# Kernel tuning notes

Hardware: AMD Instinct MI355X
Metric: run time of the kernel (lower is better)

The kernel has to match this reference:

```python
import jax, jax.numpy as jnp
import numpy as np
from jax import lax

KSIZE = 11
SIGMA = 1.5
C1 = (0.01 * 1.0) ** 2
C2 = (0.03 * 1.0) ** 2
PAD = (KSIZE - 1) // 2  # 5


def _gaussian_2d(ksize: int, sigma: float) -> np.ndarray:
    half = (ksize - 1) * 0.5
    g = np.exp(-0.5 * (np.linspace(-half, half, ksize) / sigma) ** 2)
    g = g / g.sum()
    return np.outer(g, g).astype(np.float32)  # [k, k]


def setup_inputs() -> dict:
    key = jax.random.key(0)
    kx, ky = jax.random.split(key)
    B, C, T, H, W = 2, 3, 8, 512, 512
    x = jax.random.uniform(kx, (B, C, T, H, W), dtype=jnp.float32)
    y = jax.random.uniform(ky, (B, C, T, H, W), dtype=jnp.float32)
    k2d = jnp.asarray(_gaussian_2d(KSIZE, SIGMA))
    # depthwise conv3d kernel: [C_out=C, C_in/groups=1, kD=1, kH, kW]
    kernel = jnp.broadcast_to(k2d[None, None, None], (C, 1, 1, KSIZE, KSIZE))
    return {"x": x, "y": y, "kernel": kernel}


def reference(x, y, kernel):
    C = x.shape[1]

    def conv(z):
        return lax.conv_general_dilated(
            z, kernel,
            window_strides=(1, 1, 1),
            padding=((0, 0), (PAD, PAD), (PAD, PAD)),
            dimension_numbers=("NCDHW", "OIDHW", "NCDHW"),
            feature_group_count=C,
        )

    # single grouped conv over the 5 stacked statistics, as in the original
    stacked = jnp.concatenate([x, y, x * x, y * y, x * y], axis=0)
    ux, uy, uxx, uyy, uxy = jnp.split(conv(stacked), 5, axis=0)

    vx = uxx - ux * ux
    vy = uyy - uy * uy
    vxy = uxy - ux * uy
    a1 = 2.0 * ux * uy + C1
    a2 = 2.0 * vxy + C2
    b1 = ux * ux + uy * uy + C1
    b2 = vx + vy + C2
    return a1 * a2 / (b1 * b2)
```

## Files before the change

kernel.cpp:

```cpp
#include <hip/hip_runtime.h>
#include <type_traits>

namespace {
constexpr int HH = 512;
constexpr int WW = 512;
constexpr int KS = 11;
constexpr int PADR = 5;
constexpr int TH = 32;
constexpr int TW = 64;
constexpr int SLAB = 16;
constexpr int HC = TW + 2 * PADR;
constexpr int LP = 77;
constexpr int NTHREADS = 256;
constexpr float SSIM_C1 = 1.0e-4f;
constexpr float SSIM_C2 = 9.0e-4f;
}

__global__ __launch_bounds__(NTHREADS, 4) void ssim_fused(
    const float* __restrict__ x, const float* __restrict__ y,
    const float* __restrict__ kern, float* __restrict__ out)
{
    __shared__ float vb[5][SLAB][LP];

    constexpr int tiles_w = WW / TW;
    constexpr int tiles_h = HH / TH;
    constexpr int tpp = tiles_w * tiles_h;

    const int bid = blockIdx.x;
    const int plane = bid / tpp;
    const int trem = bid - plane * tpp;
    const int tr_idx = trem / tiles_w;
    const int tile_r = tr_idx * TH;
    const int tile_c = (trem - tr_idx * tiles_w) * TW;

    const float* __restrict__ xp = x + (size_t)plane * (HH * WW);
    const float* __restrict__ yp = y + (size_t)plane * (HH * WW);
    float* __restrict__ op = out + (size_t)plane * (HH * WW);

    float wt[KS];
    {
        const float c = kern[5 * KS + 5];
        const float inv = rsqrtf(c);
#pragma unroll
        for (int i = 0; i < KS; ++i) wt[i] = kern[5 * KS + i] * inv;
    }

    const int t = threadIdx.x;
    const bool interior = (tile_r >= PADR) && (tile_r + TH + PADR <= HH) &&
                          (tile_c >= PADR) && (tile_c + TW + PADR <= WW);

    const int p2_r = t >> 4;
    const int p2_c0 = (t & 15) * 4;

    auto run_slab = [&](int s0, auto intr_tag) {
        constexpr bool INTR = decltype(intr_tag)::value;
        for (int i = t; i < SLAB * HC; i += NTHREADS) {
            const int r = i / HC;
            const int c = i - r * HC;
            const int gr = tile_r + s0 + r;
            const int gc = tile_c + c - PADR;
            float sx = 0.f, sy = 0.f, sxx = 0.f, syy = 0.f, sxy = 0.f;
            if (INTR) {
                const float* xq = xp + (gr - PADR) * WW + gc;
                const float* yq = yp + (gr - PADR) * WW + gc;
#pragma unroll
                for (int k = 0; k < KS; ++k) {
                    const float xv = xq[k * WW];
                    const float yv = yq[k * WW];
                    const float w = wt[k];
                    sx  += w * xv;
                    sy  += w * yv;
                    sxx += w * xv * xv;
                    syy += w * yv * yv;
                    sxy += w * xv * yv;
                }
            } else {
                const bool cok = (gc >= 0) & (gc < WW);
#pragma unroll
                for (int k = 0; k < KS; ++k) {
                    const int rr = gr - PADR + k;
                    const bool ok = cok & (rr >= 0) & (rr < HH);
                    float xv = 0.f, yv = 0.f;
                    if (ok) {
                        xv = xp[rr * WW + gc];
                        yv = yp[rr * WW + gc];
                    }
                    const float w = wt[k];
                    sx  += w * xv;
                    sy  += w * yv;
                    sxx += w * xv * xv;
                    syy += w * yv * yv;
                    sxy += w * xv * yv;
                }
            }
            vb[0][r][c] = sx;
            vb[1][r][c] = sy;
            vb[2][r][c] = sxx;
            vb[3][r][c] = syy;
            vb[4][r][c] = sxy;
        }
        __syncthreads();

        float res[5][4];
#pragma unroll
        for (int s = 0; s < 5; ++s) {
            float wnd[KS + 3];
#pragma unroll
            for (int i2 = 0; i2 < KS + 3; ++i2) wnd[i2] = vb[s][p2_r][p2_c0 + i2];
#pragma unroll
            for (int j = 0; j < 4; ++j) {
                float a = 0.f;
#pragma unroll
                for (int k = 0; k < KS; ++k) a += wt[k] * wnd[j + k];
                res[s][j] = a;
            }
        }
        float4 o;
#pragma unroll
        for (int j = 0; j < 4; ++j) {
            const float ux = res[0][j], uy = res[1][j];
            const float uxx = res[2][j], uyy = res[3][j], uxy = res[4][j];
            const float vx  = uxx - ux * ux;
            const float vy  = uyy - uy * uy;
            const float vxy = uxy - ux * uy;
            const float a1 = 2.f * ux * uy + SSIM_C1;
            const float a2 = 2.f * vxy + SSIM_C2;
            const float b1 = ux * ux + uy * uy + SSIM_C1;
            const float b2 = vx + vy + SSIM_C2;
            (&o.x)[j] = (a1 * a2) * __builtin_amdgcn_rcpf(b1 * b2);
        }
        *(float4*)(op + (size_t)(tile_r + s0 + p2_r) * WW + (tile_c + p2_c0)) = o;
        __syncthreads();
    };

    if (interior) {
        run_slab(0,    std::true_type{});
        run_slab(SLAB, std::true_type{});
    } else {
        run_slab(0,    std::false_type{});
        run_slab(SLAB, std::false_type{});
    }
}

extern "C" void kernel_launch(void* const* d_in, const int* in_sizes, int n_in,
                              void* d_out, int out_size, void* d_ws, size_t ws_size,
                              hipStream_t stream) {
    const float* x    = (const float*)d_in[0];
    const float* y    = (const float*)d_in[1];
    const float* kern = (const float*)d_in[2];
    float* out = (float*)d_out;

    const int nplanes = in_sizes[0] / (HH * WW);
    const int nblocks = nplanes * (HH / TH) * (WW / TW);

    ssim_fused<<<dim3(nblocks), dim3(NTHREADS), 0, stream>>>(x, y, kern, out);
}
```

Measured before the change: 227.3 us.

## Process full-width row bands with register sliding vertical blur

Blocks now each own a full-width band of 32 rows instead of a 32x64 tile. Each thread loads float2 columns and computes 8 output rows of the vertical pass from 18 input rows held in registers, so each input row is loaded once per round rather than 11 times per output. The horizontal halo is reduced to zero padding in shared memory. In exchange the grid shrinks to 768 blocks, register pressure rises (launch bounds drop to 3), and there are more barriers per block.

```diff
diff --git a/kernel.cpp b/kernel.cpp
--- a/kernel.cpp
+++ b/kernel.cpp
@@ -6,32 +6,25 @@
 constexpr int WW = 512;
 constexpr int KS = 11;
 constexpr int PADR = 5;
-constexpr int TH = 32;
-constexpr int TW = 64;
-constexpr int SLAB = 16;
-constexpr int HC = TW + 2 * PADR;
-constexpr int LP = 77;
+constexpr int BH = 32;
+constexpr int VR = 8;
+constexpr int SR = 4;
+constexpr int LP = 525;
 constexpr int NTHREADS = 256;
 constexpr float SSIM_C1 = 1.0e-4f;
 constexpr float SSIM_C2 = 9.0e-4f;
 }
 
-__global__ __launch_bounds__(NTHREADS, 4) void ssim_fused(
+__global__ __launch_bounds__(NTHREADS, 3) void ssim_fused(
     const float* __restrict__ x, const float* __restrict__ y,
     const float* __restrict__ kern, float* __restrict__ out)
 {
-    __shared__ float vb[5][SLAB][LP];
-
-    constexpr int tiles_w = WW / TW;
-    constexpr int tiles_h = HH / TH;
-    constexpr int tpp = tiles_w * tiles_h;
+    __shared__ float vb[5][SR][LP];
 
     const int bid = blockIdx.x;
-    const int plane = bid / tpp;
-    const int trem = bid - plane * tpp;
-    const int tr_idx = trem / tiles_w;
-    const int tile_r = tr_idx * TH;
-    const int tile_c = (trem - tr_idx * tiles_w) * TW;
+    const int plane = bid >> 4;
+    const int band  = bid & 15;
+    const int tile_r = band * BH;
 
     const float* __restrict__ xp = x + (size_t)plane * (HH * WW);
     const float* __restrict__ yp = y + (size_t)plane * (HH * WW);
@@ -46,99 +39,127 @@
     }
 
     const int t = threadIdx.x;
-    const bool interior = (tile_r >= PADR) && (tile_r + TH + PADR <= HH) &&
-                          (tile_c >= PADR) && (tile_c + TW + PADR <= WW);
+    const int c0 = 2 * t;
 
-    const int p2_r = t >> 4;
-    const int p2_c0 = (t & 15) * 4;
+    {
+        constexpr int PADL = PADR;
+        constexpr int PADRW = LP - (WW + PADR);
+        constexpr int PPR = PADL + PADRW;
+        for (int i = t; i < 5 * SR * PPR; i += NTHREADS) {
+            const int q = i / PPR;
+            const int rm = i - q * PPR;
+            const int col = (rm < PADL) ? rm : (WW + PADR + rm - PADL);
+            (&vb[0][0][0])[q * LP + col] = 0.f;
+        }
+    }
+    __syncthreads();
 
-    auto run_slab = [&](int s0, auto intr_tag) {
+    const bool interior = (tile_r >= PADR) && (tile_r + BH + PADR <= HH);
+
+    const int prow = (t >> 4) & 3;
+    const int pcg  = (t & 15) | ((t >> 6) << 4);
+
+    auto run_round = [&](int r0, auto intr_tag) {
         constexpr bool INTR = decltype(intr_tag)::value;
-        for (int i = t; i < SLAB * HC; i += NTHREADS) {
-            const int r = i / HC;
-            const int c = i - r * HC;
-            const int gr = tile_r + s0 + r;
-            const int gc = tile_c + c - PADR;
-            float sx = 0.f, sy = 0.f, sxx = 0.f, syy = 0.f, sxy = 0.f;
+
+        float2 acc[5][VR];
+#pragma unroll
+        for (int s = 0; s < 5; ++s)
+#pragma unroll
+            for (int o = 0; o < VR; ++o) acc[s][o] = make_float2(0.f, 0.f);
+
+        const float* xq = xp + (ptrdiff_t)(r0 - PADR) * WW + c0;
+        const float* yq = yp + (ptrdiff_t)(r0 - PADR) * WW + c0;
+#pragma unroll
+        for (int k = 0; k < VR + 2 * PADR; ++k) {
+            float2 xv, yv;
             if (INTR) {
-                const float* xq = xp + (gr - PADR) * WW + gc;
-                const float* yq = yp + (gr - PADR) * WW + gc;
-#pragma unroll
-                for (int k = 0; k < KS; ++k) {
-                    const float xv = xq[k * WW];
-                    const float yv = yq[k * WW];
-                    const float w = wt[k];
-                    sx  += w * xv;
-                    sy  += w * yv;
-                    sxx += w * xv * xv;
-                    syy += w * yv * yv;
-                    sxy += w * xv * yv;
-                }
+                xv = *(const float2*)(xq + (ptrdiff_t)k * WW);
+                yv = *(const float2*)(yq + (ptrdiff_t)k * WW);
             } else {
-                const bool cok = (gc >= 0) & (gc < WW);
-#pragma unroll
-                for (int k = 0; k < KS; ++k) {
-                    const int rr = gr - PADR + k;
-                    const bool ok = cok & (rr >= 0) & (rr < HH);
-                    float xv = 0.f, yv = 0.f;
-                    if (ok) {
-                        xv = xp[rr * WW + gc];
-                        yv = yp[rr * WW + gc];
-                    }
-                    const float w = wt[k];
-                    sx  += w * xv;
-                    sy  += w * yv;
-                    sxx += w * xv * xv;
-                    syy += w * yv * yv;
-                    sxy += w * xv * yv;
+                const int rr = r0 - PADR + k;
+                if (rr >= 0 && rr < HH) {
+                    xv = *(const float2*)(xq + (ptrdiff_t)k * WW);
+                    yv = *(const float2*)(yq + (ptrdiff_t)k * WW);
+                } else {
+                    xv = make_float2(0.f, 0.f);
+                    yv = make_float2(0.f, 0.f);
                 }
             }
-            vb[0][r][c] = sx;
-            vb[1][r][c] = sy;
-            vb[2][r][c] = sxx;
-            vb[3][r][c] = syy;
-            vb[4][r][c] = sxy;
-        }
-        __syncthreads();
-
-        float res[5][4];
+            const float xx0 = xv.x * xv.x, xx1 = xv.y * xv.y;
+            const float yy0 = yv.x * yv.x, yy1 = yv.y * yv.y;
+            const float xy0 = xv.x * yv.x, xy1 = xv.y * yv.y;
 #pragma unroll
-        for (int s = 0; s < 5; ++s) {
-            float wnd[KS + 3];
-#pragma unroll
-            for (int i2 = 0; i2 < KS + 3; ++i2) wnd[i2] = vb[s][p2_r][p2_c0 + i2];
-#pragma unroll
-            for (int j = 0; j < 4; ++j) {
-                float a = 0.f;
-#pragma unroll
-                for (int k = 0; k < KS; ++k) a += wt[k] * wnd[j + k];
-                res[s][j] = a;
+            for (int o = 0; o < VR; ++o) {
+                constexpr int dummy = 0; (void)dummy;
+                const int j = k - o;
+                if (j >= 0 && j < KS) {
+                    const float w = wt[j];
+                    acc[0][o].x += w * xv.x;  acc[0][o].y += w * xv.y;
+                    acc[1][o].x += w * yv.x;  acc[1][o].y += w * yv.y;
+                    acc[2][o].x += w * xx0;   acc[2][o].y += w * xx1;
+                    acc[3][o].x += w * yy0;   acc[3][o].y += w * yy1;
+                    acc[4][o].x += w * xy0;   acc[4][o].y += w * xy1;
+                }
             }
         }
-        float4 o;
+
 #pragma unroll
-        for (int j = 0; j < 4; ++j) {
-            const float ux = res[0][j], uy = res[1][j];
-            const float uxx = res[2][j], uyy = res[3][j], uxy = res[4][j];
-            const float vx  = uxx - ux * ux;
-            const float vy  = uyy - uy * uy;
-            const float vxy = uxy - ux * uy;
-            const float a1 = 2.f * ux * uy + SSIM_C1;
-            const float a2 = 2.f * vxy + SSIM_C2;
-            const float b1 = ux * ux + uy * uy + SSIM_C1;
-            const float b2 = vx + vy + SSIM_C2;
-            (&o.x)[j] = (a1 * a2) * __builtin_amdgcn_rcpf(b1 * b2);
+        for (int sub = 0; sub < 2; ++sub) {
+#pragma unroll
+            for (int rr = 0; rr < SR; ++rr) {
+#pragma unroll
+                for (int s = 0; s < 5; ++s) {
+                    vb[s][rr][c0 + PADR]     = acc[s][sub * SR + rr].x;
+                    vb[s][rr][c0 + PADR + 1] = acc[s][sub * SR + rr].y;
+                }
+            }
+            __syncthreads();
+
+#pragma unroll
+            for (int pass = 0; pass < 2; ++pass) {
+                const int ocol = (pcg + (pass << 6)) << 2;
+                float res[5][4];
+#pragma unroll
+                for (int s = 0; s < 5; ++s) {
+                    float wnd[KS + 3];
+#pragma unroll
+                    for (int i2 = 0; i2 < KS + 3; ++i2)
+                        wnd[i2] = vb[s][prow][ocol + i2];
+#pragma unroll
+                    for (int jj = 0; jj < 4; ++jj) {
+                        float a = 0.f;
+#pragma unroll
+                        for (int k = 0; k < KS; ++k) a += wt[k] * wnd[jj + k];
+                        res[s][jj] = a;
+                    }
+                }
+                float4 o4;
+#pragma unroll
+                for (int jj = 0; jj < 4; ++jj) {
+                    const float ux = res[0][jj], uy = res[1][jj];
+                    const float uxx = res[2][jj], uyy = res[3][jj], uxy = res[4][jj];
+                    const float vx  = uxx - ux * ux;
+                    const float vy  = uyy - uy * uy;
+                    const float vxy = uxy - ux * uy;
+                    const float a1 = 2.f * ux * uy + SSIM_C1;
+                    const float a2 = 2.f * vxy + SSIM_C2;
+                    const float b1 = ux * ux + uy * uy + SSIM_C1;
+                    const float b2 = vx + vy + SSIM_C2;
+                    (&o4.x)[jj] = (a1 * a2) * __builtin_amdgcn_rcpf(b1 * b2);
+                }
+                *(float4*)(op + (size_t)(r0 + sub * SR + prow) * WW + ocol) = o4;
+            }
+            __syncthreads();
         }
-        *(float4*)(op + (size_t)(tile_r + s0 + p2_r) * WW + (tile_c + p2_c0)) = o;
-        __syncthreads();
     };
 
     if (interior) {
-        run_slab(0,    std::true_type{});
-        run_slab(SLAB, std::true_type{});
+        for (int j = 0; j < BH / VR; ++j)
+            run_round(tile_r + j * VR, std::true_type{});
     } else {
-        run_slab(0,    std::false_type{});
-        run_slab(SLAB, std::false_type{});
+        for (int j = 0; j < BH / VR; ++j)
+            run_round(tile_r + j * VR, std::false_type{});
     }
 }
 
@@ -151,7 +172,7 @@
     float* out = (float*)d_out;
 
     const int nplanes = in_sizes[0] / (HH * WW);
-    const int nblocks = nplanes * (HH / TH) * (WW / TW);
+    const int nblocks = nplanes * (HH / BH);
 
     ssim_fused<<<dim3(nblocks), dim3(NTHREADS), 0, stream>>>(x, y, kern, out);
 }
```

Result: slower. 570.9 us (+151.2%).
